# Kernel optimization log

Hardware: AMD Instinct MI355X
Metric: run time of the kernel (lower is better)

The kernel has to match this reference:

```python
import jax, jax.numpy as jnp
import numpy as np


def setup_inputs() -> dict:
    key = jax.random.key(0)
    ks = jax.random.split(key, 16)
    B, C, H, W = 2, 64, 512, 512
    Nl, Nr = 100000, 20000

    def lin(k, fan_in, fan_out):
        kw, kb = jax.random.split(k)
        bound = 1.0 / np.sqrt(fan_in)
        w = jax.random.uniform(kw, (fan_in, fan_out), jnp.float32, -bound, bound)
        b = jax.random.uniform(kb, (fan_out,), jnp.float32, -bound, bound)
        return w, b

    w_lin, b_lin = lin(ks[0], 128, 64)
    w1, b1 = lin(ks[1], 128, 64)
    w2, b2 = lin(ks[2], 64, 32)
    w3, b3 = lin(ks[3], 32, 16)
    w4, b4 = lin(ks[4], 16, 1)

    return {
        "pc0_map": jax.random.normal(ks[5], (B, C, H, W), jnp.float32),
        "pc1_map": jax.random.normal(ks[6], (B, C, H, W), jnp.float32),
        "flow_map": jax.random.normal(ks[7], (B, C, H, W), jnp.float32),
        "lidar_coords": jax.random.randint(ks[8], (B, Nl, 3), 0, 512).astype(jnp.int64),
        "radar_coords": jax.random.randint(ks[9], (B, Nr, 3), 0, 512).astype(jnp.int64),
        "w_lin": w_lin, "b_lin": b_lin,
        "w1": w1, "b1": b1, "w2": w2, "b2": b2,
        "w3": w3, "b3": b3, "w4": w4, "b4": b4,
    }


def reference(pc0_map, pc1_map, flow_map, lidar_coords, radar_coords,
              w_lin, b_lin, w1, b1, w2, b2, w3, b3, w4, b4):
    gelu = lambda x: jax.nn.gelu(x, approximate=False)  # torch nn.GELU default (erf)

    def seg_single(p0, p1, fl, lc, rc):
        # lc: [Nl,3], rc: [Nr,3]; cat(lidar, radar) for all three maps
        coords = jnp.concatenate([lc, rc], axis=0)        # [N,3]
        r, c = coords[:, 1], coords[:, 2]
        f0 = p0[:, r, c].T                                # [N,64]
        f1 = p1[:, r, c].T                                # [N,64]
        ff = fl[:, r, c].T                                # [N,64]
        pc = jnp.concatenate([f0, f1], axis=1) @ w_lin + b_lin   # [N,64]
        h = jnp.concatenate([pc, ff], axis=1)             # [N,128]
        h = gelu(h @ w1 + b1)
        h = gelu(h @ w2 + b2)
        h = gelu(h @ w3 + b3)
        s = jax.nn.sigmoid(h @ w4 + b4)                   # [N,1]
        return s[:, 0]

    # [B, Nl+Nr] stacked (original returns a per-batch list; fixed N lets us stack)
    return jax.vmap(seg_single)(pc0_map, pc1_map, flow_map, lidar_coords, radar_coords)
```

## Files before the change

### kernel.cpp

```cpp
#include <hip/hip_runtime.h>
#include <math.h>

#define NPTS 120000
#define NLID 100000
#define NRAD 20000
#define NTOT (2 * NPTS)
#define MAPW 512
#define MAPHW (512 * 512)
#define NBINS 16384

typedef short sh8 __attribute__((ext_vector_type(8)));
typedef float f32x4 __attribute__((ext_vector_type(4)));
typedef unsigned short u16;
typedef unsigned int u32;

#define FROW 65
#define H1S 72
#define H2S 40
#define H3S 24
#define HWAVE (16 * (H1S + H2S + H3S))

__device__ __forceinline__ float gelu_f(float x) {
    return 0.5f * x * (1.0f + erff(x * 0.7071067811865476f));
}
__device__ __forceinline__ u16 f2bf(float f) {
    unsigned int u = __float_as_uint(f);
    return (u16)((u + 0x7FFFu + ((u >> 16) & 1u)) >> 16);
}
__device__ __forceinline__ float bf2f(u16 h) {
    return __uint_as_float((unsigned int)h << 16);
}

__device__ __forceinline__ void point_rc(int p, const int* __restrict__ lidar,
                                         const int* __restrict__ radar,
                                         int& b, int& r, int& c) {
    b = p / NPTS;
    int i = p - b * NPTS;
    if (i < NLID) {
        const int* cd = lidar + (size_t)(b * NLID + i) * 3;
        r = cd[1]; c = cd[2];
    } else {
        const int* cd = radar + (size_t)(b * NRAD + (i - NLID)) * 3;
        r = cd[1]; c = cd[2];
    }
}
__device__ __forceinline__ int bin_key(int b, int r, int c) {
    return (b << 13) | (r << 4) | (c >> 5);
}
__global__ void hist_kernel(const int* __restrict__ lidar, const int* __restrict__ radar,
                            int* __restrict__ hist) {
    int p = blockIdx.x * blockDim.x + threadIdx.x;
    if (p >= NTOT) return;
    int b, r, c; point_rc(p, lidar, radar, b, r, c);
    atomicAdd(&hist[bin_key(b, r, c)], 1);
}
__global__ __launch_bounds__(1024) void scan_kernel(const int* __restrict__ hist,
                                                    int* __restrict__ offs) {
    __shared__ int sums[1024];
    const int t = threadIdx.x;
    int local[16]; int s = 0;
    #pragma unroll
    for (int i = 0; i < 16; i++) { local[i] = hist[t * 16 + i]; s += local[i]; }
    sums[t] = s;
    __syncthreads();
    for (int off = 1; off < 1024; off <<= 1) {
        int add = (t >= off) ? sums[t - off] : 0;
        __syncthreads();
        sums[t] += add;
        __syncthreads();
    }
    int excl = (t == 0) ? 0 : sums[t - 1];
    #pragma unroll
    for (int i = 0; i < 16; i++) { offs[t * 16 + i] = excl; excl += local[i]; }
}
__global__ void scatter_kernel(const int* __restrict__ lidar, const int* __restrict__ radar,
                               int* __restrict__ offs, int2* __restrict__ sorted) {
    int p = blockIdx.x * blockDim.x + threadIdx.x;
    if (p >= NTOT) return;
    int b, r, c; point_rc(p, lidar, radar, b, r, c);
    int pos = atomicAdd(&offs[bin_key(b, r, c)], 1);
    sorted[pos] = make_int2(p, (r << 9) | c);
}

__global__ void wprep_kernel(const float* __restrict__ w_lin, const float* __restrict__ b_lin,
                             const float* __restrict__ w1, const float* __restrict__ b1,
                             const float* __restrict__ w2, const float* __restrict__ w3,
                             u16* __restrict__ wfrag1, u16* __restrict__ wfrag2,
                             u16* __restrict__ wfrag3, float* __restrict__ b_eff) {
    int e = blockIdx.x * blockDim.x + threadIdx.x;
    if (e < 12288) {
        int fi = e >> 9, r = e & 511, lane = r >> 3, j = r & 7;
        int kk = fi >> 2, nt = fi & 3;
        int k = kk * 32 + (lane >> 4) * 8 + j;
        int n = nt * 16 + (lane & 15);
        float val;
        if (k < 128) {
            float s = 0.f;
            for (int jj = 0; jj < 64; jj++) s += w_lin[k * 64 + jj] * w1[jj * 64 + n];
            val = s;
        } else {
            val = w1[(k - 64) * 64 + n];
        }
        wfrag1[e] = f2bf(val);
    } else if (e < 12288 + 2048) {
        int e2 = e - 12288;
        int fi = e2 >> 9, lane = (e2 >> 3) & 63, j = e2 & 7;
        int kk = fi >> 1, nt = fi & 1;
        int k = kk * 32 + (lane >> 4) * 8 + j;
        int n = nt * 16 + (lane & 15);
        wfrag2[e2] = f2bf(w2[k * 32 + n]);
    } else if (e < 12288 + 2048 + 512) {
        int e3 = e - 12288 - 2048;
        int lane = e3 >> 3, j = e3 & 7;
        int k = (lane >> 4) * 8 + j;
        int n = lane & 15;
        wfrag3[e3] = f2bf(w3[k * 16 + n]);
    } else if (e < 12288 + 2048 + 512 + 64) {
        int n = e - 12288 - 2048 - 512;
        float s = b1[n];
        for (int jj = 0; jj < 64; jj++) s += b_lin[jj] * w1[jj * 64 + n];
        b_eff[n] = s;
    }
}

__global__ __launch_bounds__(256) void fbseg_kernel(
    const float* __restrict__ p0, const float* __restrict__ p1,
    const float* __restrict__ fl,
    const int2* __restrict__ sorted,
    const u16* __restrict__ wfrag1, const u16* __restrict__ wfrag2,
    const u16* __restrict__ wfrag3, const float* __restrict__ b_eff,
    const float* __restrict__ b2, const float* __restrict__ b3,
    const float* __restrict__ w4, const float* __restrict__ b4,
    float* __restrict__ out)
{
    __shared__ __align__(16) float smem[192 * FROW];

    const int tid = threadIdx.x;
    const int wv = tid >> 6;
    const int lane = tid & 63;
    const int p_base = blockIdx.x * 64;

    {
        const int2 e = sorted[p_base + lane];
        const int b = e.x / NPTS;
        const int r = (e.y >> 9) & 511;
        const int c = e.y & 511;
        const size_t off = (size_t)b * ((size_t)64 * MAPHW) + (size_t)r * MAPW + (size_t)c;
        const float* bases[3] = {p0 + off, p1 + off, fl + off};
        #pragma unroll
        for (int m = 0; m < 3; m++) {
            const float* gp = bases[m] + (size_t)wv * MAPHW;
            #pragma unroll
            for (int u = 0; u < 16; u++) {
                const int chu = __builtin_amdgcn_readfirstlane(m * 64 + u * 4 + wv);
                __builtin_amdgcn_global_load_lds(
                    (const __attribute__((address_space(1))) u32*)gp,
                    (__attribute__((address_space(3))) u32*)(&smem[chu * FROW]),
                    4, 0, 0);
                gp += (size_t)4 * MAPHW;
            }
        }
    }
    __syncthreads();

    const int m0 = wv * 16;
    const int lr = lane & 15;
    const int lq = lane >> 4;
    const int col = m0 + lr;

    f32x4 acc1[4] = {};
    #pragma unroll
    for (int kk = 0; kk < 6; kk++) {
        sh8 a;
        u16* ap = (u16*)&a;
        #pragma unroll
        for (int j = 0; j < 8; j++)
            ap[j] = f2bf(smem[(kk * 32 + lq * 8 + j) * FROW + col]);
        #pragma unroll
        for (int nt = 0; nt < 4; nt++) {
            sh8 bfr = *(const sh8*)(wfrag1 + ((kk * 4 + nt) * 64 + lane) * 8);
            acc1[nt] = __builtin_amdgcn_mfma_f32_16x16x32_bf16(a, bfr, acc1[nt], 0, 0, 0);
        }
    }
    __syncthreads();

    u16* Hbase = (u16*)smem + wv * HWAVE;
    u16* H1w = Hbase;
    u16* H2w = Hbase + 16 * H1S;
    u16* H3w = Hbase + 16 * H1S + 16 * H2S;

    #pragma unroll
    for (int nt = 0; nt < 4; nt++) {
        const int n = nt * 16 + lr;
        const float bias = b_eff[n];
        #pragma unroll
        for (int rg = 0; rg < 4; rg++) {
            const int row = lq * 4 + rg;
            H1w[row * H1S + n] = f2bf(gelu_f(acc1[nt][rg] + bias));
        }
    }

    f32x4 acc2[2] = {};
    #pragma unroll
    for (int kk = 0; kk < 2; kk++) {
        sh8 a = *(const sh8*)&H1w[lr * H1S + kk * 32 + lq * 8];
        #pragma unroll
        for (int nt = 0; nt < 2; nt++) {
            sh8 bfr = *(const sh8*)(wfrag2 + ((kk * 2 + nt) * 64 + lane) * 8);
            acc2[nt] = __builtin_amdgcn_mfma_f32_16x16x32_bf16(a, bfr, acc2[nt], 0, 0, 0);
        }
    }
    #pragma unroll
    for (int nt = 0; nt < 2; nt++) {
        const int n = nt * 16 + lr;
        const float bias = b2[n];
        #pragma unroll
        for (int rg = 0; rg < 4; rg++) {
            const int row = lq * 4 + rg;
            H2w[row * H2S + n] = f2bf(gelu_f(acc2[nt][rg] + bias));
        }
    }

    f32x4 acc3 = {};
    {
        sh8 a = *(const sh8*)&H2w[lr * H2S + lq * 8];
        sh8 bfr = *(const sh8*)(wfrag3 + lane * 8);
        acc3 = __builtin_amdgcn_mfma_f32_16x16x32_bf16(a, bfr, acc3, 0, 0, 0);
    }
    {
        const float bias = b3[lr];
        #pragma unroll
        for (int rg = 0; rg < 4; rg++) {
            const int row = lq * 4 + rg;
            H3w[row * H3S + lr] = f2bf(gelu_f(acc3[rg] + bias));
        }
    }

    if (lane < 16) {
        float s = b4[0];
        #pragma unroll
        for (int k = 0; k < 16; k++) s = fmaf(bf2f(H3w[lane * H3S + k]), w4[k], s);
        const int orig = sorted[p_base + m0 + lane].x;
        out[orig] = 1.0f / (1.0f + expf(-s));
    }
}

extern "C" void kernel_launch(void* const* d_in, const int* in_sizes, int n_in,
                              void* d_out, int out_size, void* d_ws, size_t ws_size,
                              hipStream_t stream) {
    const float* p0    = (const float*)d_in[0];
    const float* p1    = (const float*)d_in[1];
    const float* fl    = (const float*)d_in[2];
    const int*   lidar = (const int*)d_in[3];
    const int*   radar = (const int*)d_in[4];
    const float* w_lin = (const float*)d_in[5];
    const float* b_lin = (const float*)d_in[6];
    const float* w1    = (const float*)d_in[7];
    const float* b1    = (const float*)d_in[8];
    const float* w2    = (const float*)d_in[9];
    const float* b2    = (const float*)d_in[10];
    const float* w3    = (const float*)d_in[11];
    const float* b3    = (const float*)d_in[12];
    const float* w4    = (const float*)d_in[13];
    const float* b4    = (const float*)d_in[14];
    float* out = (float*)d_out;

    char* ws = (char*)d_ws;
    int*  hist   = (int*)ws;
    int*  offs   = (int*)(ws + NBINS * sizeof(int));
    int2* sorted = (int2*)(ws + 2 * NBINS * sizeof(int));
    char* wbase  = ws + 2 * NBINS * sizeof(int) + (size_t)NTOT * sizeof(int2);
    u16*  wfrag1 = (u16*)wbase;
    u16*  wfrag2 = (u16*)(wbase + 12288 * 2);
    u16*  wfrag3 = (u16*)(wbase + (12288 + 2048) * 2);
    float* b_eff = (float*)(wbase + (12288 + 2048 + 512) * 2);

    hipMemsetAsync(hist, 0, NBINS * sizeof(int), stream);
    hipLaunchKernelGGL(hist_kernel, dim3((NTOT + 255) / 256), dim3(256), 0, stream,
                       lidar, radar, hist);
    hipLaunchKernelGGL(scan_kernel, dim3(1), dim3(1024), 0, stream, hist, offs);
    hipLaunchKernelGGL(scatter_kernel, dim3((NTOT + 255) / 256), dim3(256), 0, stream,
                       lidar, radar, offs, sorted);
    hipLaunchKernelGGL(wprep_kernel, dim3((14912 + 255) / 256), dim3(256), 0, stream,
                       w_lin, b_lin, w1, b1, w2, w3, wfrag1, wfrag2, wfrag3, b_eff);
    hipLaunchKernelGGL(fbseg_kernel, dim3(NTOT / 64), dim3(256), 0, stream,
                       p0, p1, fl, sorted, wfrag1, wfrag2, wfrag3, b_eff,
                       b2, b3, w4, b4, out);
}
```

Measured before the change: 422.7 us.

## Evaluate MLP densely over all pixels and look up per-point scores

Instead of sorting points into bins and gathering scattered per-point features, the kernel computes the segmentation score for every pixel of both batch maps using coalesced 16-byte global-to-LDS loads. A small lookup kernel then reads each point's score from the dense score map. This removes the histogram, scan and scatter kernels and the poorly coalesced 4-byte gathers, at the cost of reading all map data and running the MLP on about twice as many positions.

```diff
diff --git a/kernel.cpp b/kernel.cpp
--- a/kernel.cpp
+++ b/kernel.cpp
@@ -7,14 +7,13 @@
 #define NTOT (2 * NPTS)
 #define MAPW 512
 #define MAPHW (512 * 512)
-#define NBINS 16384
 
 typedef short sh8 __attribute__((ext_vector_type(8)));
 typedef float f32x4 __attribute__((ext_vector_type(4)));
 typedef unsigned short u16;
 typedef unsigned int u32;
 
-#define FROW 65
+#define GSTR 264
 #define H1S 72
 #define H2S 40
 #define H3S 24
@@ -29,57 +28,6 @@
 }
 __device__ __forceinline__ float bf2f(u16 h) {
     return __uint_as_float((unsigned int)h << 16);
-}
-
-__device__ __forceinline__ void point_rc(int p, const int* __restrict__ lidar,
-                                         const int* __restrict__ radar,
-                                         int& b, int& r, int& c) {
-    b = p / NPTS;
-    int i = p - b * NPTS;
-    if (i < NLID) {
-        const int* cd = lidar + (size_t)(b * NLID + i) * 3;
-        r = cd[1]; c = cd[2];
-    } else {
-        const int* cd = radar + (size_t)(b * NRAD + (i - NLID)) * 3;
-        r = cd[1]; c = cd[2];
-    }
-}
-__device__ __forceinline__ int bin_key(int b, int r, int c) {
-    return (b << 13) | (r << 4) | (c >> 5);
-}
-__global__ void hist_kernel(const int* __restrict__ lidar, const int* __restrict__ radar,
-                            int* __restrict__ hist) {
-    int p = blockIdx.x * blockDim.x + threadIdx.x;
-    if (p >= NTOT) return;
-    int b, r, c; point_rc(p, lidar, radar, b, r, c);
-    atomicAdd(&hist[bin_key(b, r, c)], 1);
-}
-__global__ __launch_bounds__(1024) void scan_kernel(const int* __restrict__ hist,
-                                                    int* __restrict__ offs) {
-    __shared__ int sums[1024];
-    const int t = threadIdx.x;
-    int local[16]; int s = 0;
-    #pragma unroll
-    for (int i = 0; i < 16; i++) { local[i] = hist[t * 16 + i]; s += local[i]; }
-    sums[t] = s;
-    __syncthreads();
-    for (int off = 1; off < 1024; off <<= 1) {
-        int add = (t >= off) ? sums[t - off] : 0;
-        __syncthreads();
-        sums[t] += add;
-        __syncthreads();
-    }
-    int excl = (t == 0) ? 0 : sums[t - 1];
-    #pragma unroll
-    for (int i = 0; i < 16; i++) { offs[t * 16 + i] = excl; excl += local[i]; }
-}
-__global__ void scatter_kernel(const int* __restrict__ lidar, const int* __restrict__ radar,
-                               int* __restrict__ offs, int2* __restrict__ sorted) {
-    int p = blockIdx.x * blockDim.x + threadIdx.x;
-    if (p >= NTOT) return;
-    int b, r, c; point_rc(p, lidar, radar, b, r, c);
-    int pos = atomicAdd(&offs[bin_key(b, r, c)], 1);
-    sorted[pos] = make_int2(p, (r << 9) | c);
 }
 
 __global__ void wprep_kernel(const float* __restrict__ w_lin, const float* __restrict__ b_lin,
@@ -123,41 +71,43 @@
     }
 }
 
-__global__ __launch_bounds__(256) void fbseg_kernel(
+__global__ __launch_bounds__(256) void fbseg_dense_kernel(
     const float* __restrict__ p0, const float* __restrict__ p1,
     const float* __restrict__ fl,
-    const int2* __restrict__ sorted,
     const u16* __restrict__ wfrag1, const u16* __restrict__ wfrag2,
     const u16* __restrict__ wfrag3, const float* __restrict__ b_eff,
     const float* __restrict__ b2, const float* __restrict__ b3,
     const float* __restrict__ w4, const float* __restrict__ b4,
-    float* __restrict__ out)
+    float* __restrict__ score)
 {
-    __shared__ __align__(16) float smem[192 * FROW];
+    __shared__ __align__(16) float smem[48 * GSTR];
 
     const int tid = threadIdx.x;
     const int wv = tid >> 6;
     const int lane = tid & 63;
-    const int p_base = blockIdx.x * 64;
+
+    const int nb = blockIdx.x;
+    const int b  = nb >> 12;
+    const int r  = (nb & 4095) >> 3;
+    const int c0 = (nb & 7) << 6;
 
     {
-        const int2 e = sorted[p_base + lane];
-        const int b = e.x / NPTS;
-        const int r = (e.y >> 9) & 511;
-        const int c = e.y & 511;
-        const size_t off = (size_t)b * ((size_t)64 * MAPHW) + (size_t)r * MAPW + (size_t)c;
+        const size_t off = (size_t)b * ((size_t)64 * MAPHW)
+                         + (size_t)r * MAPW + (size_t)c0
+                         + (size_t)(lane >> 4) * MAPHW
+                         + (size_t)((lane & 15) * 4);
         const float* bases[3] = {p0 + off, p1 + off, fl + off};
         #pragma unroll
         for (int m = 0; m < 3; m++) {
-            const float* gp = bases[m] + (size_t)wv * MAPHW;
             #pragma unroll
-            for (int u = 0; u < 16; u++) {
-                const int chu = __builtin_amdgcn_readfirstlane(m * 64 + u * 4 + wv);
+            for (int u = 0; u < 4; u++) {
+                const int g = u * 4 + wv;
+                const int G = __builtin_amdgcn_readfirstlane(m * 16 + g);
+                const float* gp = bases[m] + (size_t)(g * 4) * MAPHW;
                 __builtin_amdgcn_global_load_lds(
                     (const __attribute__((address_space(1))) u32*)gp,
-                    (__attribute__((address_space(3))) u32*)(&smem[chu * FROW]),
-                    4, 0, 0);
-                gp += (size_t)4 * MAPHW;
+                    (__attribute__((address_space(3))) u32*)(&smem[G * GSTR]),
+                    16, 0, 0);
             }
         }
     }
@@ -174,8 +124,10 @@
         sh8 a;
         u16* ap = (u16*)&a;
         #pragma unroll
-        for (int j = 0; j < 8; j++)
-            ap[j] = f2bf(smem[(kk * 32 + lq * 8 + j) * FROW + col]);
+        for (int j = 0; j < 8; j++) {
+            const int k = kk * 32 + lq * 8 + j;
+            ap[j] = f2bf(smem[(k >> 2) * GSTR + (k & 3) * 64 + col]);
+        }
         #pragma unroll
         for (int nt = 0; nt < 4; nt++) {
             sh8 bfr = *(const sh8*)(wfrag1 + ((kk * 4 + nt) * 64 + lane) * 8);
@@ -240,9 +192,26 @@
         float s = b4[0];
         #pragma unroll
         for (int k = 0; k < 16; k++) s = fmaf(bf2f(H3w[lane * H3S + k]), w4[k], s);
-        const int orig = sorted[p_base + m0 + lane].x;
-        out[orig] = 1.0f / (1.0f + expf(-s));
-    }
+        score[(size_t)b * MAPHW + (size_t)r * MAPW + (size_t)(c0 + m0 + lane)] =
+            1.0f / (1.0f + expf(-s));
+    }
+}
+
+__global__ void lookup_kernel(const int* __restrict__ lidar, const int* __restrict__ radar,
+                              const float* __restrict__ score, float* __restrict__ out) {
+    int p = blockIdx.x * blockDim.x + threadIdx.x;
+    if (p >= NTOT) return;
+    int b = p / NPTS;
+    int i = p - b * NPTS;
+    int r, c;
+    if (i < NLID) {
+        const int* cd = lidar + (size_t)(b * NLID + i) * 3;
+        r = cd[1]; c = cd[2];
+    } else {
+        const int* cd = radar + (size_t)(b * NRAD + (i - NLID)) * 3;
+        r = cd[1]; c = cd[2];
+    }
+    out[p] = score[(size_t)b * MAPHW + (size_t)r * MAPW + (size_t)c];
 }
 
 extern "C" void kernel_launch(void* const* d_in, const int* in_sizes, int n_in,
@@ -266,24 +235,17 @@
     float* out = (float*)d_out;
 
     char* ws = (char*)d_ws;
-    int*  hist   = (int*)ws;
-    int*  offs   = (int*)(ws + NBINS * sizeof(int));
-    int2* sorted = (int2*)(ws + 2 * NBINS * sizeof(int));
-    char* wbase  = ws + 2 * NBINS * sizeof(int) + (size_t)NTOT * sizeof(int2);
+    float* score = (float*)ws;
+    char* wbase  = ws + (size_t)2 * MAPHW * sizeof(float);
     u16*  wfrag1 = (u16*)wbase;
     u16*  wfrag2 = (u16*)(wbase + 12288 * 2);
     u16*  wfrag3 = (u16*)(wbase + (12288 + 2048) * 2);
     float* b_eff = (float*)(wbase + (12288 + 2048 + 512) * 2);
 
-    hipMemsetAsync(hist, 0, NBINS * sizeof(int), stream);
-    hipLaunchKernelGGL(hist_kernel, dim3((NTOT + 255) / 256), dim3(256), 0, stream,
-                       lidar, radar, hist);
-    hipLaunchKernelGGL(scan_kernel, dim3(1), dim3(1024), 0, stream, hist, offs);
-    hipLaunchKernelGGL(scatter_kernel, dim3((NTOT + 255) / 256), dim3(256), 0, stream,
-                       lidar, radar, offs, sorted);
     hipLaunchKernelGGL(wprep_kernel, dim3((14912 + 255) / 256), dim3(256), 0, stream,
                        w_lin, b_lin, w1, b1, w2, w3, wfrag1, wfrag2, wfrag3, b_eff);
-    hipLaunchKernelGGL(fbseg_kernel, dim3(NTOT / 64), dim3(256), 0, stream,
-                       p0, p1, fl, sorted, wfrag1, wfrag2, wfrag3, b_eff,
-                       b2, b3, w4, b4, out);
-}
+    hipLaunchKernelGGL(fbseg_dense_kernel, dim3(8192), dim3(256), 0, stream,
+                       p0, p1, fl, wfrag1, wfrag2, wfrag3, b_eff, b2, b3, w4, b4, score);
+    hipLaunchKernelGGL(lookup_kernel, dim3((NTOT + 255) / 256), dim3(256), 0, stream,
+                       lidar, radar, score, out);
+}
```

Result: faster. 407.9 us (-3.5%).
